# Kernel optimization log

Measured on AMD Instinct MI355X. Metric: run time of the kernel, lower is better.

Reference implementation:

```python
import jax, jax.numpy as jnp
import numpy as np

N = 50000      # nodes
E = 800000     # edges
NF = 128       # node_features
BF = 16        # bond_features
H = 4          # heads
C = 32         # hidden_size (per-head out channels)
HC = H * C     # 128 == NF, so all GAT layers share weight shape
DEPTH = 5
NEG_SLOPE = 0.2


def _sanitize(t):
    return jnp.nan_to_num(t, nan=0.0, posinf=1000.0, neginf=-1000.0)


def setup_inputs() -> dict:
    key = jax.random.key(0)
    ks = jax.random.split(key, 12)
    s = 0.1
    x = jax.random.normal(ks[0], (N, NF), jnp.float32)
    edge_index = jax.random.randint(ks[1], (2, E), 0, N, dtype=jnp.int32)
    edge_attr = jax.random.uniform(ks[2], (E, BF), jnp.float32)
    W = jax.random.normal(ks[3], (DEPTH, NF, HC), jnp.float32) * s
    att_src = jax.random.normal(ks[4], (DEPTH, H, C), jnp.float32) * s
    att_dst = jax.random.normal(ks[5], (DEPTH, H, C), jnp.float32) * s
    We = jax.random.normal(ks[6], (DEPTH, BF, HC), jnp.float32) * s
    att_edge = jax.random.normal(ks[7], (DEPTH, H, C), jnp.float32) * s
    b = jnp.zeros((DEPTH, HC), jnp.float32)
    Wout = jax.random.normal(ks[8], (NF + HC, C), jnp.float32) * s
    bout = jnp.zeros((C,), jnp.float32)
    return {"x": x, "edge_index": edge_index, "edge_attr": edge_attr,
            "W": W, "att_src": att_src, "att_dst": att_dst,
            "We": We, "att_edge": att_edge, "b": b,
            "Wout": Wout, "bout": bout}


def _gat_layer(h, s2, d2, ea, W_l, as_l, ad_l, We_l, ae_l, b_l):
    # h: [N, in_dim]; s2/d2: [E+N] edges incl. self loops; ea: [E+N, BF]
    xp = (h @ W_l).reshape(N, H, C)                     # lin(x), view per-head
    a_s = jnp.sum(xp * as_l, axis=-1)                   # [N, H]
    a_d = jnp.sum(xp * ad_l, axis=-1)                   # [N, H]
    ee = (ea @ We_l).reshape(-1, H, C)                  # lin_edge(edge_attr)
    a_e = jnp.sum(ee * ae_l, axis=-1)                   # [E+N, H]
    alpha = jax.nn.leaky_relu(a_s[s2] + a_d[d2] + a_e, NEG_SLOPE)
    # segment softmax over edges grouped by destination node
    m = jax.ops.segment_max(alpha, d2, num_segments=N)  # every node has a self loop -> finite
    ex = jnp.exp(alpha - m[d2])
    den = jax.ops.segment_sum(ex, d2, num_segments=N)
    coef = ex / (den[d2] + 1e-16)                       # [E+N, H]
    out = jax.ops.segment_sum(coef[:, :, None] * xp[s2], d2, num_segments=N)
    return out.reshape(N, HC) + b_l


def reference(x, edge_index, edge_attr, W, att_src, att_dst, We, att_edge, b, Wout, bout):
    src, dst = edge_index[0], edge_index[1]
    # add self loops with fill_value='mean': self-loop attr = mean of incoming edge_attr
    deg = jax.ops.segment_sum(jnp.ones((E,), edge_attr.dtype), dst, num_segments=N)
    sl_attr = jax.ops.segment_sum(edge_attr, dst, num_segments=N) / jnp.maximum(deg, 1.0)[:, None]
    ea = jnp.concatenate([edge_attr, sl_attr], axis=0)          # [E+N, BF]
    loop = jnp.arange(N, dtype=src.dtype)
    s2 = jnp.concatenate([src, loop])
    d2 = jnp.concatenate([dst, loop])

    h = _sanitize(x)
    for l in range(DEPTH):
        h = _gat_layer(h, s2, d2, ea, W[l], att_src[l], att_dst[l], We[l], att_edge[l], b[l])
        h = jax.nn.relu(h)            # dropout is a no-op in eval mode
        h = _sanitize(h)
    h_cat = jnp.concatenate([x, h], axis=1)             # [N, NF+HC]
    out = jax.nn.relu(h_cat @ Wout + bout)
    return _sanitize(out)
```

## Files before the change

kernel.cpp:

```cpp
#include <hip/hip_runtime.h>

#define NN 50000
#define NE 800000
#define NF 128
#define BF 16
#define NH 4
#define HC 128
#define CC 32
#define DEPTH 5
#define NEG 0.2f
#define NPART 256
#define PTILE 4096

typedef __attribute__((ext_vector_type(8))) short bf16x8;
typedef __attribute__((ext_vector_type(4))) float f32x4;

__device__ inline unsigned short f2bf(float f) {
  union { float f; unsigned u; } v; v.f = f;
  unsigned r = v.u + 0x7fff + ((v.u >> 16) & 1);
  return (unsigned short)(r >> 16);
}
__device__ inline float bf2f(unsigned short u) {
  union { unsigned u; float f; } v; v.u = (unsigned)u << 16; return v.f;
}

__global__ __launch_bounds__(256) void k_cnt0(const int* __restrict__ edst,
                                              int* __restrict__ deg,
                                              int* __restrict__ pcnt) {
  __shared__ int lc[NPART];
  int t = threadIdx.x;
  lc[t] = 0;
  __syncthreads();
  int base = blockIdx.x * PTILE;
#pragma unroll
  for (int j = 0; j < PTILE / 256; ++j) {
    int e = base + t + j * 256;
    if (e < NE) {
      int d = edst[e];
      atomicAdd(&deg[d], 1);
      atomicAdd(&lc[d >> 8], 1);
    }
  }
  __syncthreads();
  if (lc[t]) atomicAdd(&pcnt[t], lc[t]);
}

__global__ void k_partial(const int* __restrict__ deg, int* __restrict__ bsum) {
  __shared__ int s[256];
  int t = threadIdx.x;
  int i = blockIdx.x * 256 + t;
  s[t] = (i < NN) ? deg[i] : 0;
  __syncthreads();
  for (int d = 128; d > 0; d >>= 1) {
    if (t < d) s[t] += s[t + d];
    __syncthreads();
  }
  if (t == 0) bsum[blockIdx.x] = s[0];
}

__global__ void k_scan_top(int* __restrict__ bsum, int nb) {
  if (threadIdx.x == 0 && blockIdx.x == 0) {
    int run = 0;
    for (int i = 0; i < nb; ++i) { int v = bsum[i]; bsum[i] = run; run += v; }
  }
}

__global__ void k_scan_write(const int* __restrict__ deg, const int* __restrict__ bsum,
                             int* __restrict__ offs, int* __restrict__ cur) {
  __shared__ int s[256];
  int t = threadIdx.x;
  int i = blockIdx.x * 256 + t;
  int v = (i < NN) ? deg[i] : 0;
  s[t] = v;
  __syncthreads();
  for (int d = 1; d < 256; d <<= 1) {
    int x = (t >= d) ? s[t - d] : 0;
    __syncthreads();
    s[t] += x;
    __syncthreads();
  }
  if (i < NN) {
    int o = bsum[blockIdx.x] + s[t] - v;
    offs[i] = o;
    cur[i] = o;
  }
  if (i == 0) offs[NN] = NE;
}

__global__ void k_pscan(const int* __restrict__ pcnt, int* __restrict__ pbase,
                        int* __restrict__ pcur) {
  __shared__ int s[NPART];
  int t = threadIdx.x;
  int v = pcnt[t];
  s[t] = v;
  __syncthreads();
  for (int d = 1; d < NPART; d <<= 1) {
    int x = (t >= d) ? s[t - d] : 0;
    __syncthreads();
    s[t] += x;
    __syncthreads();
  }
  int ex = s[t] - v;
  pbase[t] = ex;
  pcur[t] = ex;
  if (t == NPART - 1) pbase[NPART] = s[NPART - 1];
}

__global__ __launch_bounds__(256) void k_p1(const int* __restrict__ edst,
                                            int* __restrict__ pcur,
                                            int2* __restrict__ staging) {
  __shared__ int lc[NPART];
  __shared__ int lbase[NPART];
  __shared__ int lrank[NPART];
  int t = threadIdx.x;
  lc[t] = 0;
  __syncthreads();
  int base = blockIdx.x * PTILE;
  int myd[PTILE / 256];
#pragma unroll
  for (int j = 0; j < PTILE / 256; ++j) {
    int e = base + t + j * 256;
    int d = (e < NE) ? edst[e] : -1;
    myd[j] = d;
    if (d >= 0) atomicAdd(&lc[d >> 8], 1);
  }
  __syncthreads();
  if (lc[t]) lbase[t] = atomicAdd(&pcur[t], lc[t]);
  lrank[t] = 0;
  __syncthreads();
#pragma unroll
  for (int j = 0; j < PTILE / 256; ++j) {
    int d = myd[j];
    if (d >= 0) {
      int p = d >> 8;
      int r = atomicAdd(&lrank[p], 1);
      staging[lbase[p] + r] = make_int2(base + t + j * 256, d);
    }
  }
}

__global__ __launch_bounds__(256) void k_p2(const int2* __restrict__ staging,
                                            const int* __restrict__ pbase,
                                            int* __restrict__ cur,
                                            int* __restrict__ csr_eid) {
  int p = blockIdx.x;
  int s = pbase[p], e = pbase[p + 1];
  for (int i = s + threadIdx.x; i < e; i += 256) {
    int2 st = staging[i];
    int slot = atomicAdd(&cur[st.y], 1);
    csr_eid[slot] = st.x;
  }
}

__global__ void k_weff(const float* __restrict__ We, const float* __restrict__ ae,
                       float* __restrict__ weff) {
  int idx = threadIdx.x;
  if (idx >= DEPTH * BF * NH) return;
  int l = idx / (BF * NH);
  int r = idx - l * (BF * NH);
  int f = r >> 2, h = r & 3;
  const float* We_l = We + (size_t)l * BF * HC;
  const float* ae_l = ae + (size_t)l * NH * CC;
  float acc = 0.f;
  for (int c = 0; c < CC; ++c) acc += We_l[f * HC + h * CC + c] * ae_l[h * CC + c];
  weff[idx] = acc;
}

__global__ __launch_bounds__(256) void k_aeprep(const int* __restrict__ csr_eid,
                                                const int* __restrict__ esrc,
                                                const float* __restrict__ eattr,
                                                const float* __restrict__ weff,
                                                unsigned short* __restrict__ ae_csr,
                                                int* __restrict__ csr_src) {
  __shared__ float sw[DEPTH * BF * NH];
  int t = threadIdx.x;
  if (t < DEPTH * BF * NH) sw[t] = weff[t];
  __syncthreads();
  int i = blockIdx.x * 256 + t;
  if (i >= NE) return;
  int eid = csr_eid[i];
  csr_src[i] = esrc[eid];
  float at[16];
  const float4* ar = (const float4*)(eattr + (size_t)eid * BF);
#pragma unroll
  for (int q = 0; q < 4; ++q) {
    float4 v = ar[q];
    at[q * 4] = v.x; at[q * 4 + 1] = v.y; at[q * 4 + 2] = v.z; at[q * 4 + 3] = v.w;
  }
#pragma unroll
  for (int l = 0; l < DEPTH; ++l) {
    float a0 = 0.f, a1 = 0.f, a2 = 0.f, a3 = 0.f;
#pragma unroll
    for (int f = 0; f < BF; ++f) {
      float av = at[f];
      const float* wf = &sw[(l * BF + f) * NH];
      a0 += av * wf[0]; a1 += av * wf[1]; a2 += av * wf[2]; a3 += av * wf[3];
    }
    ushort4 u;
    u.x = f2bf(a0); u.y = f2bf(a1); u.z = f2bf(a2); u.w = f2bf(a3);
    ((ushort4*)ae_csr)[(size_t)l * NE + i] = u;
  }
}

__global__ void k_aeself(const unsigned short* __restrict__ ae_csr,
                         const int* __restrict__ offs,
                         unsigned short* __restrict__ ae_self) {
  int idx = blockIdx.x * 256 + threadIdx.x;
  if (idx >= NN * DEPTH) return;
  int l = idx / NN, n = idx - l * NN;
  int s = offs[n], e = offs[n + 1];
  const ushort4* base = (const ushort4*)ae_csr + (size_t)l * NE;
  float a0 = 0.f, a1 = 0.f, a2 = 0.f, a3 = 0.f;
  for (int i = s; i < e; ++i) {
    ushort4 u = base[i];
    a0 += bf2f(u.x); a1 += bf2f(u.y); a2 += bf2f(u.z); a3 += bf2f(u.w);
  }
  float inv = 1.0f / fmaxf((float)(e - s), 1.0f);
  ushort4 o;
  o.x = f2bf(a0 * inv); o.y = f2bf(a1 * inv); o.z = f2bf(a2 * inv); o.w = f2bf(a3 * inv);
  ((ushort4*)ae_self)[(size_t)l * NN + n] = o;
}

__global__ void k_x2bf(const float* __restrict__ x, unsigned short* __restrict__ xb) {
  int i = blockIdx.x * 256 + threadIdx.x;
  if (i >= NN * 32) return;
  float4 v = ((const float4*)x)[i];
  ushort4 u;
  u.x = f2bf(v.x); u.y = f2bf(v.y); u.z = f2bf(v.z); u.w = f2bf(v.w);
  ((ushort4*)xb)[i] = u;
}

__global__ void k_wprep(const float* __restrict__ W, unsigned short* __restrict__ Wt) {
  int idx = blockIdx.x * 256 + threadIdx.x;
  if (idx >= DEPTH * NF * HC) return;
  int l = idx >> 14;
  int rem = idx & 16383;
  int n = rem >> 7, k = rem & 127;
  Wt[(size_t)l * 16384 + (size_t)n * 128 + k] = f2bf(W[(size_t)l * 16384 + (size_t)k * 128 + n]);
}

__global__ __launch_bounds__(256) void k_gemm_mfma(const unsigned short* __restrict__ Ab,
                                                   const unsigned short* __restrict__ Wt,
                                                   const float* __restrict__ as_w,
                                                   const float* __restrict__ ad_w,
                                                   unsigned short* __restrict__ xpb,
                                                   float* __restrict__ a_s,
                                                   float* __restrict__ a_d) {
  __shared__ unsigned short cl[128][144];
  __shared__ float swS[128], dwS[128];
  int t = threadIdx.x;
  if (t < 128) { swS[t] = as_w[t]; dwS[t] = ad_w[t]; }
  int wv = t >> 6;
  int l = t & 63;
  int r0 = blockIdx.x * 128;
  int lk = (l >> 4) * 8;
  int c0 = wv * 32;
  f32x4 acc[8][2] = {};
#pragma unroll
  for (int ks = 0; ks < 4; ++ks) {
    int kb = ks * 32 + lk;
    bf16x8 bfr0 = *(const bf16x8*)&Wt[(size_t)(c0 + (l & 15)) * 128 + kb];
    bf16x8 bfr1 = *(const bf16x8*)&Wt[(size_t)(c0 + 16 + (l & 15)) * 128 + kb];
#pragma unroll
    for (int rt = 0; rt < 8; ++rt) {
      int row = r0 + rt * 16 + (l & 15);
      row = row < NN ? row : NN - 1;
      bf16x8 afr = *(const bf16x8*)&Ab[(size_t)row * 128 + kb];
      acc[rt][0] = __builtin_amdgcn_mfma_f32_16x16x32_bf16(afr, bfr0, acc[rt][0], 0, 0, 0);
      acc[rt][1] = __builtin_amdgcn_mfma_f32_16x16x32_bf16(afr, bfr1, acc[rt][1], 0, 0, 0);
    }
  }
#pragma unroll
  for (int rt = 0; rt < 8; ++rt) {
#pragma unroll
    for (int j = 0; j < 4; ++j) {
      int lr = rt * 16 + (l >> 4) * 4 + j;
      cl[lr][c0 + (l & 15)] = f2bf(acc[rt][0][j]);
      cl[lr][c0 + 16 + (l & 15)] = f2bf(acc[rt][1][j]);
    }
  }
  __syncthreads();
  int row = t >> 1;
  int grow = r0 + row;
  int p = t & 1;
  if (grow < NN) {
    uint4* dst = (uint4*)&xpb[(size_t)grow * 128];
#pragma unroll
    for (int q = 0; q < 8; ++q)
      dst[q * 2 + p] = *(uint4*)&cl[row][(q * 2 + p) * 8];
  }
  int row2 = t >> 2;
  int hh = t & 3;
  int hc = hh * 32;
#pragma unroll
  for (int half = 0; half < 2; ++half) {
    int rr = row2 + half * 64;
    int gr = r0 + rr;
    float ps = 0.f, pd = 0.f;
#pragma unroll
    for (int q = 0; q < 4; ++q) {
      uint4 u = *(uint4*)&cl[rr][hc + q * 8];
      const unsigned short* us = (const unsigned short*)&u;
#pragma unroll
      for (int k = 0; k < 8; ++k) {
        float xv = bf2f(us[k]);
        ps += xv * swS[hc + q * 8 + k];
        pd += xv * dwS[hc + q * 8 + k];
      }
    }
    if (gr < NN) {
      a_s[(size_t)gr * 4 + hh] = ps;
      a_d[(size_t)gr * 4 + hh] = pd;
    }
  }
}

__global__ __launch_bounds__(256) void k_aggr(const unsigned short* __restrict__ xpb,
                                              const unsigned short* __restrict__ ae_l,
                                              const unsigned short* __restrict__ aeself_l,
                                              const float* __restrict__ a_s,
                                              const float* __restrict__ a_d,
                                              const int* __restrict__ csr_src,
                                              const int* __restrict__ offs,
                                              const float* __restrict__ b_l,
                                              unsigned short* __restrict__ hout) {
  int node = blockIdx.x * 4 + (threadIdx.x >> 6);
  if (node >= NN) return;
  int lane = threadIdx.x & 63;
  int q = lane & 15;
  int h = lane >> 4;
  int base = lane & 48;
  const ushort2* xp2 = (const ushort2*)xpb;
  int s = offs[node], e = offs[node + 1];
  float ad = a_d[(size_t)node * 4 + h];
  float vs = a_s[(size_t)node * 4 + h] + ad + bf2f(aeself_l[(size_t)node * 4 + h]);
  vs = vs > 0.f ? vs : NEG * vs;
  float es = __expf(fminf(vs, 60.f));
  ushort2 xs = xp2[(size_t)node * 64 + lane];
  float acc0 = es * bf2f(xs.x), acc1 = es * bf2f(xs.y);
  float den = es;
  for (int i = s; i < e; i += 16) {
    int cnt = e - i;
    int srcv = 0;
    float w = 0.f;
    if (q < cnt) {
      srcv = csr_src[i + q];
      float a = a_s[(size_t)srcv * 4 + h] + ad + bf2f(ae_l[(size_t)(i + q) * 4 + h]);
      a = a > 0.f ? a : NEG * a;
      w = __expf(fminf(a, 60.f));
    }
#pragma unroll 8
    for (int qq = 0; qq < 16; ++qq) {
      int sq = __shfl(srcv, base | qq);
      float wq = __shfl(w, base | qq);
      ushort2 xq = xp2[(size_t)sq * 64 + lane];
      den += wq;
      acc0 += wq * bf2f(xq.x);
      acc1 += wq * bf2f(xq.y);
    }
  }
  float2 b2 = ((const float2*)b_l)[lane];
  float inv = 1.0f / (den + 1e-16f);
  float o0 = fmaxf(acc0 * inv + b2.x, 0.f);
  float o1 = fmaxf(acc1 * inv + b2.y, 0.f);
  ushort2 ho;
  ho.x = f2bf(o0); ho.y = f2bf(o1);
  ((ushort2*)hout)[(size_t)node * 64 + lane] = ho;
}

__global__ __launch_bounds__(256) void k_final(const float* __restrict__ x,
                                               const unsigned short* __restrict__ h,
                                               const float* __restrict__ Wout, const float* __restrict__ bout,
                                               float* __restrict__ out) {
  __shared__ float4 wlds[2048];
  int t = threadIdx.x;
#pragma unroll
  for (int i = 0; i < 8; ++i) wlds[t + i * 256] = ((const float4*)Wout)[t + i * 256];
  __syncthreads();
  int tx = t & 7;
  int ty = t >> 3;
  int row0 = blockIdx.x * 64 + ty;
  int row1 = row0 + 32;
  bool v0 = row0 < NN, v1 = row1 < NN;
  const float4* x4 = (const float4*)x;
  const ushort4* h4 = (const ushort4*)h;
  float acc[2][4] = {};
  const float4 z = make_float4(0.f, 0.f, 0.f, 0.f);
#pragma unroll 4
  for (int k4 = 0; k4 < 32; ++k4) {
    float4 a0 = v0 ? x4[(size_t)row0 * 32 + k4] : z;
    float4 a1 = v1 ? x4[(size_t)row1 * 32 + k4] : z;
    float av0[4] = {a0.x, a0.y, a0.z, a0.w};
    float av1[4] = {a1.x, a1.y, a1.z, a1.w};
#pragma unroll
    for (int kk = 0; kk < 4; ++kk) {
      float4 w = wlds[(k4 * 4 + kk) * 8 + tx];
      acc[0][0] += av0[kk] * w.x; acc[0][1] += av0[kk] * w.y;
      acc[0][2] += av0[kk] * w.z; acc[0][3] += av0[kk] * w.w;
      acc[1][0] += av1[kk] * w.x; acc[1][1] += av1[kk] * w.y;
      acc[1][2] += av1[kk] * w.z; acc[1][3] += av1[kk] * w.w;
    }
  }
#pragma unroll 4
  for (int k4 = 0; k4 < 32; ++k4) {
    ushort4 u0 = v0 ? h4[(size_t)row0 * 32 + k4] : make_ushort4(0, 0, 0, 0);
    ushort4 u1 = v1 ? h4[(size_t)row1 * 32 + k4] : make_ushort4(0, 0, 0, 0);
    float av0[4] = {bf2f(u0.x), bf2f(u0.y), bf2f(u0.z), bf2f(u0.w)};
    float av1[4] = {bf2f(u1.x), bf2f(u1.y), bf2f(u1.z), bf2f(u1.w)};
#pragma unroll
    for (int kk = 0; kk < 4; ++kk) {
      float4 w = wlds[(128 + k4 * 4 + kk) * 8 + tx];
      acc[0][0] += av0[kk] * w.x; acc[0][1] += av0[kk] * w.y;
      acc[0][2] += av0[kk] * w.z; acc[0][3] += av0[kk] * w.w;
      acc[1][0] += av1[kk] * w.x; acc[1][1] += av1[kk] * w.y;
      acc[1][2] += av1[kk] * w.z; acc[1][3] += av1[kk] * w.w;
    }
  }
  float4 b4 = ((const float4*)bout)[tx];
  if (v0) {
    float4 o = make_float4(fmaxf(acc[0][0] + b4.x, 0.f), fmaxf(acc[0][1] + b4.y, 0.f),
                           fmaxf(acc[0][2] + b4.z, 0.f), fmaxf(acc[0][3] + b4.w, 0.f));
    ((float4*)out)[(size_t)row0 * 8 + tx] = o;
  }
  if (v1) {
    float4 o = make_float4(fmaxf(acc[1][0] + b4.x, 0.f), fmaxf(acc[1][1] + b4.y, 0.f),
                           fmaxf(acc[1][2] + b4.z, 0.f), fmaxf(acc[1][3] + b4.w, 0.f));
    ((float4*)out)[(size_t)row1 * 8 + tx] = o;
  }
}

extern "C" void kernel_launch(void* const* d_in, const int* in_sizes, int n_in,
                              void* d_out, int out_size, void* d_ws, size_t ws_size,
                              hipStream_t stream) {
  const float* x        = (const float*)d_in[0];
  const int*   eidx     = (const int*)d_in[1];
  const float* eattr    = (const float*)d_in[2];
  const float* W        = (const float*)d_in[3];
  const float* att_src  = (const float*)d_in[4];
  const float* att_dst  = (const float*)d_in[5];
  const float* We       = (const float*)d_in[6];
  const float* att_edge = (const float*)d_in[7];
  const float* b        = (const float*)d_in[8];
  const float* Wout     = (const float*)d_in[9];
  const float* bout     = (const float*)d_in[10];
  float* out = (float*)d_out;

  const int* esrc = eidx;
  const int* edst = eidx + NE;

  size_t off = 0;
  auto carve = [&](size_t bytes) {
    void* p = (char*)d_ws + off;
    off += (bytes + 255) & ~(size_t)255;
    return p;
  };
  unsigned short* h_buf   = (unsigned short*)carve((size_t)NN * HC * 2);
  unsigned short* xpb     = (unsigned short*)carve((size_t)NN * HC * 2);
  unsigned short* Wt      = (unsigned short*)carve((size_t)DEPTH * NF * HC * 2);
  unsigned short* ae_csr  = (unsigned short*)carve((size_t)DEPTH * NE * NH * 2);
  unsigned short* ae_self = (unsigned short*)carve((size_t)DEPTH * NN * NH * 2);
  float* a_s   = (float*)carve((size_t)NN * NH * 4);
  float* a_d   = (float*)carve((size_t)NN * NH * 4);
  float* weff  = (float*)carve((size_t)DEPTH * BF * NH * 4);
  int* deg  = (int*)carve((size_t)NN * 4);
  int* offs = (int*)carve((size_t)(NN + 1) * 4);
  int* cur  = (int*)carve((size_t)NN * 4);
  int2* staging = (int2*)carve((size_t)NE * 8);
  int* csr_eid = (int*)carve((size_t)NE * 4);
  int* csr_src = (int*)carve((size_t)NE * 4);
  int* pcnt  = (int*)carve((size_t)NPART * 4);
  int* pbase = (int*)carve((size_t)(NPART + 1) * 4);
  int* pcur  = (int*)carve((size_t)NPART * 4);
  int* bsum = (int*)carve(1024);

  const int nbN = (NN + 255) / 256;
  const int nbE = (NE + 255) / 256;
  const int nbP = (NE + PTILE - 1) / PTILE;

  hipMemsetAsync(deg, 0, (size_t)NN * 4, stream);
  hipMemsetAsync(pcnt, 0, (size_t)NPART * 4, stream);
  k_cnt0<<<nbP, 256, 0, stream>>>(edst, deg, pcnt);
  k_partial<<<nbN, 256, 0, stream>>>(deg, bsum);
  k_scan_top<<<1, 64, 0, stream>>>(bsum, nbN);
  k_scan_write<<<nbN, 256, 0, stream>>>(deg, bsum, offs, cur);
  k_pscan<<<1, NPART, 0, stream>>>(pcnt, pbase, pcur);
  k_p1<<<nbP, 256, 0, stream>>>(edst, pcur, staging);
  k_p2<<<NPART, 256, 0, stream>>>(staging, pbase, cur, csr_eid);
  k_weff<<<1, 320, 0, stream>>>(We, att_edge, weff);
  k_aeprep<<<nbE, 256, 0, stream>>>(csr_eid, esrc, eattr, weff, ae_csr, csr_src);
  k_aeself<<<(NN * DEPTH + 255) / 256, 256, 0, stream>>>(ae_csr, offs, ae_self);
  k_x2bf<<<(NN * 32 + 255) / 256, 256, 0, stream>>>(x, h_buf);
  k_wprep<<<(DEPTH * NF * HC + 255) / 256, 256, 0, stream>>>(W, Wt);

  for (int l = 0; l < DEPTH; ++l) {
    k_gemm_mfma<<<(NN + 127) / 128, 256, 0, stream>>>(h_buf, Wt + (size_t)l * NF * HC,
                                                      att_src + (size_t)l * NH * CC,
                                                      att_dst + (size_t)l * NH * CC,
                                                      xpb, a_s, a_d);
    k_aggr<<<(NN + 3) / 4, 256, 0, stream>>>(xpb,
                                             ae_csr + (size_t)l * NE * NH,
                                             ae_self + (size_t)l * NN * NH,
                                             a_s, a_d, csr_src, offs,
                                             b + (size_t)l * HC, h_buf);
  }
  k_final<<<(NN + 63) / 64, 256, 0, stream>>>(x, h_buf, Wout, bout, out);
}
```

Measured before the change: 474.4 us.

## Compute per-node CSR offsets inside partition kernel, drop global degree scan

```diff
diff --git a/kernel.cpp b/kernel.cpp
--- a/kernel.cpp
+++ b/kernel.cpp
@@ -11,6 +11,7 @@
 #define NEG 0.2f
 #define NPART 256
 #define PTILE 4096
+#define CTILE 1024
 
 typedef __attribute__((ext_vector_type(8))) short bf16x8;
 typedef __attribute__((ext_vector_type(4))) float f32x4;
@@ -24,71 +25,24 @@
   union { unsigned u; float f; } v; v.u = (unsigned)u << 16; return v.f;
 }
 
-__global__ __launch_bounds__(256) void k_cnt0(const int* __restrict__ edst,
-                                              int* __restrict__ deg,
+__global__ __launch_bounds__(256) void k_hist(const int* __restrict__ edst,
                                               int* __restrict__ pcnt) {
   __shared__ int lc[NPART];
   int t = threadIdx.x;
   lc[t] = 0;
   __syncthreads();
-  int base = blockIdx.x * PTILE;
-#pragma unroll
-  for (int j = 0; j < PTILE / 256; ++j) {
+  int base = blockIdx.x * CTILE;
+#pragma unroll
+  for (int j = 0; j < CTILE / 256; ++j) {
     int e = base + t + j * 256;
-    if (e < NE) {
-      int d = edst[e];
-      atomicAdd(&deg[d], 1);
-      atomicAdd(&lc[d >> 8], 1);
-    }
+    if (e < NE) atomicAdd(&lc[edst[e] >> 8], 1);
   }
   __syncthreads();
   if (lc[t]) atomicAdd(&pcnt[t], lc[t]);
 }
 
-__global__ void k_partial(const int* __restrict__ deg, int* __restrict__ bsum) {
-  __shared__ int s[256];
-  int t = threadIdx.x;
-  int i = blockIdx.x * 256 + t;
-  s[t] = (i < NN) ? deg[i] : 0;
-  __syncthreads();
-  for (int d = 128; d > 0; d >>= 1) {
-    if (t < d) s[t] += s[t + d];
-    __syncthreads();
-  }
-  if (t == 0) bsum[blockIdx.x] = s[0];
-}
-
-__global__ void k_scan_top(int* __restrict__ bsum, int nb) {
-  if (threadIdx.x == 0 && blockIdx.x == 0) {
-    int run = 0;
-    for (int i = 0; i < nb; ++i) { int v = bsum[i]; bsum[i] = run; run += v; }
-  }
-}
-
-__global__ void k_scan_write(const int* __restrict__ deg, const int* __restrict__ bsum,
-                             int* __restrict__ offs, int* __restrict__ cur) {
-  __shared__ int s[256];
-  int t = threadIdx.x;
-  int i = blockIdx.x * 256 + t;
-  int v = (i < NN) ? deg[i] : 0;
-  s[t] = v;
-  __syncthreads();
-  for (int d = 1; d < 256; d <<= 1) {
-    int x = (t >= d) ? s[t - d] : 0;
-    __syncthreads();
-    s[t] += x;
-    __syncthreads();
-  }
-  if (i < NN) {
-    int o = bsum[blockIdx.x] + s[t] - v;
-    offs[i] = o;
-    cur[i] = o;
-  }
-  if (i == 0) offs[NN] = NE;
-}
-
 __global__ void k_pscan(const int* __restrict__ pcnt, int* __restrict__ pbase,
-                        int* __restrict__ pcur) {
+                        int* __restrict__ pcur, int* __restrict__ offs) {
   __shared__ int s[NPART];
   int t = threadIdx.x;
   int v = pcnt[t];
@@ -103,7 +57,10 @@
   int ex = s[t] - v;
   pbase[t] = ex;
   pcur[t] = ex;
-  if (t == NPART - 1) pbase[NPART] = s[NPART - 1];
+  if (t == NPART - 1) {
+    pbase[NPART] = s[NPART - 1];
+    offs[NN] = NE;
+  }
 }
 
 __global__ __launch_bounds__(256) void k_p1(const int* __restrict__ edst,
@@ -141,13 +98,34 @@
 
 __global__ __launch_bounds__(256) void k_p2(const int2* __restrict__ staging,
                                             const int* __restrict__ pbase,
-                                            int* __restrict__ cur,
+                                            int* __restrict__ offs,
                                             int* __restrict__ csr_eid) {
-  int p = blockIdx.x;
+  __shared__ int ldeg[256];
+  __shared__ int lofs[256];
+  __shared__ int lcur[256];
+  int p = blockIdx.x, t = threadIdx.x;
   int s = pbase[p], e = pbase[p + 1];
-  for (int i = s + threadIdx.x; i < e; i += 256) {
+  ldeg[t] = 0;
+  __syncthreads();
+  for (int i = s + t; i < e; i += 256) atomicAdd(&ldeg[staging[i].y & 255], 1);
+  __syncthreads();
+  int v = ldeg[t];
+  lofs[t] = v;
+  __syncthreads();
+  for (int d = 1; d < 256; d <<= 1) {
+    int x = (t >= d) ? lofs[t - d] : 0;
+    __syncthreads();
+    lofs[t] += x;
+    __syncthreads();
+  }
+  int myofs = s + lofs[t] - v;
+  int node = p * 256 + t;
+  if (node < NN) offs[node] = myofs;
+  lcur[t] = myofs;
+  __syncthreads();
+  for (int i = s + t; i < e; i += 256) {
     int2 st = staging[i];
-    int slot = atomicAdd(&cur[st.y], 1);
+    int slot = atomicAdd(&lcur[st.y & 255], 1);
     csr_eid[slot] = st.x;
   }
 }
@@ -462,30 +440,23 @@
   float* a_s   = (float*)carve((size_t)NN * NH * 4);
   float* a_d   = (float*)carve((size_t)NN * NH * 4);
   float* weff  = (float*)carve((size_t)DEPTH * BF * NH * 4);
-  int* deg  = (int*)carve((size_t)NN * 4);
   int* offs = (int*)carve((size_t)(NN + 1) * 4);
-  int* cur  = (int*)carve((size_t)NN * 4);
   int2* staging = (int2*)carve((size_t)NE * 8);
   int* csr_eid = (int*)carve((size_t)NE * 4);
   int* csr_src = (int*)carve((size_t)NE * 4);
   int* pcnt  = (int*)carve((size_t)NPART * 4);
   int* pbase = (int*)carve((size_t)(NPART + 1) * 4);
   int* pcur  = (int*)carve((size_t)NPART * 4);
-  int* bsum = (int*)carve(1024);
-
-  const int nbN = (NN + 255) / 256;
+
   const int nbE = (NE + 255) / 256;
   const int nbP = (NE + PTILE - 1) / PTILE;
-
-  hipMemsetAsync(deg, 0, (size_t)NN * 4, stream);
+  const int nbC = (NE + CTILE - 1) / CTILE;
+
   hipMemsetAsync(pcnt, 0, (size_t)NPART * 4, stream);
-  k_cnt0<<<nbP, 256, 0, stream>>>(edst, deg, pcnt);
-  k_partial<<<nbN, 256, 0, stream>>>(deg, bsum);
-  k_scan_top<<<1, 64, 0, stream>>>(bsum, nbN);
-  k_scan_write<<<nbN, 256, 0, stream>>>(deg, bsum, offs, cur);
-  k_pscan<<<1, NPART, 0, stream>>>(pcnt, pbase, pcur);
+  k_hist<<<nbC, 256, 0, stream>>>(edst, pcnt);
+  k_pscan<<<1, NPART, 0, stream>>>(pcnt, pbase, pcur, offs);
   k_p1<<<nbP, 256, 0, stream>>>(edst, pcur, staging);
-  k_p2<<<NPART, 256, 0, stream>>>(staging, pbase, cur, csr_eid);
+  k_p2<<<NPART, 256, 0, stream>>>(staging, pbase, offs, csr_eid);
   k_weff<<<1, 320, 0, stream>>>(We, att_edge, weff);
   k_aeprep<<<nbE, 256, 0, stream>>>(csr_eid, esrc, eattr, weff, ae_csr, csr_src);
   k_aeself<<<(NN * DEPTH + 255) / 256, 256, 0, stream>>>(ae_csr, offs, ae_self);
```

New measurement: 420.9 us. 1.13x faster.
